# Performance work log

Measured on AMD Instinct MI355X. Metric: run time of the kernel, lower is better.

The kernel has to match this reference:

```python
import jax, jax.numpy as jnp
import numpy as np
import math

# ---- hyperparameters (init_kwargs) ----
D = 2              # spatial dimension
MTOT = 65          # quadrature nodes per dimension (odd)
LENGTHSCALE = 0.1  # SE kernel lengthscale
OUTPUTSCALE = 1.0  # SE kernel variance
SIGMASQ = 0.05     # observation noise variance
CG_ITERS = 30      # fixed CG iteration count (replaces tol-based early stopping)
N_TRAIN = 100000
N_TEST = 50000
TWO_PI = 2.0 * math.pi


def setup_inputs() -> dict:
    key = jax.random.key(0)
    k1, k2, k3 = jax.random.split(key, 3)
    x = jax.random.uniform(k1, (N_TRAIN, D), dtype=jnp.float32)
    y = jax.random.normal(k2, (N_TRAIN,), dtype=jnp.float32)
    x_new = jax.random.uniform(k3, (N_TEST, D), dtype=jnp.float32)
    return {"x": x, "y": y, "x_new": x_new}


def _phases(col, h, freqs, isign):
    # exp(isign * i * 2*pi*h * x * k), shape [N, K]
    return jnp.exp((1j * isign * TWO_PI) * (h * col[:, None] * freqs[None, :]).astype(jnp.float32))


def _nudft_type1(pts, c, h, freqs):
    # fk[a,b] = sum_n c_n exp(-2*pi*i*h*(k_a x_n0 + k_b x_n1)); separable tensor grid
    E0 = _phases(pts[:, 0], h, freqs, -1.0)
    E1 = _phases(pts[:, 1], h, freqs, -1.0)
    return jnp.einsum('n,na,nb->ab', c.astype(jnp.complex64), E0, E1)


def _nudft_type2(pts, fk, h, freqs):
    # f_n = sum_{a,b} fk[a,b] exp(+2*pi*i*h*(k_a x_n0 + k_b x_n1))
    E0 = _phases(pts[:, 0], h, freqs, +1.0)
    E1 = _phases(pts[:, 1], h, freqs, +1.0)
    return jnp.einsum('ab,na,nb->n', fk, E0, E1)


def _cg(A, b, iters):
    # complex Hermitian-PSD conjugate gradients, fixed iteration count
    x0 = jnp.zeros_like(b)
    r0 = b
    rs0 = jnp.real(jnp.vdot(r0, r0))

    def step(carry, _):
        xk, r, p, rs = carry
        Ap = A(p)
        alpha = rs / jnp.real(jnp.vdot(p, Ap))
        xk = xk + alpha * p
        r = r - alpha * Ap
        rs_new = jnp.real(jnp.vdot(r, r))
        p = r + (rs_new / rs) * p
        return (xk, r, p, rs_new), None

    (xk, _, _, _), _ = jax.lax.scan(step, (x0, r0, r0, rs0), None, length=iters)
    return xk


def _forward(x, y, x_new):
    m = (MTOT - 1) // 2
    # geometry / quadrature (get_xis): domain extent L, spacing h = 1/L, grid k = -m..m
    x_all = jnp.concatenate((x, x_new), axis=0)
    L = jnp.max(jnp.max(x_all, axis=0) - jnp.min(x_all, axis=0))
    L = jnp.where(L <= 1e-9, jnp.float32(1.0), L)
    h = (1.0 / L).astype(jnp.float32)
    k = (jnp.arange(MTOT) - m).astype(jnp.float32)
    xis_1d = h * k
    X0, X1 = jnp.meshgrid(xis_1d, xis_1d, indexing='ij')
    sq = X0 * X0 + X1 * X1  # [MTOT, MTOT] squared frequency norm
    # squared-exponential spectral density S(s) = sigma_f^2 (2*pi*l^2)^(d/2) exp(-2*pi^2*l^2 |s|^2)
    l2 = LENGTHSCALE * LENGTHSCALE
    spec = OUTPUTSCALE * (TWO_PI * l2) ** (D / 2) * jnp.exp((-2.0 * math.pi ** 2 * l2) * sq)
    ws = jnp.sqrt(spec * h ** D).reshape(-1).astype(jnp.complex64)  # [M]

    # rhs = ws * F^H y  (type-1 NUFFT, exact NUDFT)
    rhs = ws * _nudft_type1(x, y, h, k).reshape(-1)

    # Toeplitz convolution vector v[o] = sum_n exp(-2*pi*i*h*o.x_n), offsets -(mtot-1)..(mtot-1)
    kk = (jnp.arange(2 * MTOT - 1) - (MTOT - 1)).astype(jnp.float32)
    Ev0 = _phases(x[:, 0], h, kk, -1.0)
    Ev1 = _phases(x[:, 1], h, kk, -1.0)
    v = jnp.einsum('na,nb->ab', Ev0, Ev1)  # [2M-1, 2M-1]
    # circularly align offset 0 to index 0, precompute FFT
    v_circ = jnp.roll(v, shift=(-(MTOT - 1), -(MTOT - 1)), axis=(0, 1))
    vhat = jnp.fft.fftn(v_circ)
    s_fft = (2 * MTOT - 1, 2 * MTOT - 1)

    def toeplitz_apply(w):  # w: [MTOT, MTOT] complex
        W = jnp.fft.fftn(w, s=s_fft)
        full = jnp.fft.ifftn(vhat * W)
        return full[:MTOT, :MTOT]

    def A_mean(beta):  # (W F^H F W + sigma^2 I) beta, beta flat [M]
        wb = (ws * beta).reshape(MTOT, MTOT)
        Tw = toeplitz_apply(wb).reshape(-1)
        return ws * Tw + SIGMASQ * beta

    beta = _cg(A_mean, rhs, CG_ITERS)
    # posterior mean at test points via type-2 NUFFT
    yhat = jnp.real(_nudft_type2(x_new, (ws * beta).reshape(MTOT, MTOT), h, k))
    return yhat


def reference(x, y, x_new):
    return _forward(x, y, x_new)
```

## Files before the change

### kernel.cpp

```cpp
#include <hip/hip_runtime.h>
#include <math.h>

#define M2 4225
#define NTRAIN 100000
#define NTEST 50000
#define CGITERS 30
#define TWO_PI_D 6.283185307179586476925287
#define TPI32 6.28318530717958647692f

#define F_H 0
#define F_RS 1
#define F_PAP 2
#define F_RSN 3
#define F_WS 8
#define F_RHS 4234
#define F_X 12684
#define F_R 21134
#define F_P 29584
#define F_AP 38034
#define F_PB 46484
#define F_VF 50710
#define F_VHAT 83992
#define F_PROD 117274
#define D_VPART 125330
#define D_FKPART 2271890

#define NCHUNK 128
#define PTSB2 782
#define VHALF 8385
#define VH2 16770
#define FKHALF 2145
#define FH2 4290
#define NB_APPLY 529

__device__ __forceinline__ unsigned fkey(float f){
  unsigned u = __float_as_uint(f);
  return (u & 0x80000000u) ? ~u : (u | 0x80000000u);
}
__device__ __forceinline__ float fdec(unsigned k){
  unsigned u = (k & 0x80000000u) ? (k & 0x7fffffffu) : ~k;
  return __uint_as_float(u);
}

__global__ void k_init(unsigned* mm){
  if (threadIdx.x == 0){
    mm[0] = 0xFFFFFFFFu; mm[1] = 0u; mm[2] = 0xFFFFFFFFu; mm[3] = 0u;
  }
}

__global__ void k_minmax(const float* __restrict__ x, const float* __restrict__ xn,
                         unsigned* __restrict__ mm){
  int tid = blockIdx.x * blockDim.x + threadIdx.x;
  int str = gridDim.x * blockDim.x;
  float mn0 = 1e30f, mx0 = -1e30f, mn1 = 1e30f, mx1 = -1e30f;
  const float2* a = (const float2*)x;
  for (int i = tid; i < NTRAIN; i += str){
    float2 v = a[i];
    mn0 = fminf(mn0, v.x); mx0 = fmaxf(mx0, v.x);
    mn1 = fminf(mn1, v.y); mx1 = fmaxf(mx1, v.y);
  }
  const float2* b = (const float2*)xn;
  for (int i = tid; i < NTEST; i += str){
    float2 v = b[i];
    mn0 = fminf(mn0, v.x); mx0 = fmaxf(mx0, v.x);
    mn1 = fminf(mn1, v.y); mx1 = fmaxf(mx1, v.y);
  }
  for (int off = 32; off; off >>= 1){
    mn0 = fminf(mn0, __shfl_xor(mn0, off, 64));
    mx0 = fmaxf(mx0, __shfl_xor(mx0, off, 64));
    mn1 = fminf(mn1, __shfl_xor(mn1, off, 64));
    mx1 = fmaxf(mx1, __shfl_xor(mx1, off, 64));
  }
  if ((threadIdx.x & 63) == 0){
    atomicMin(&mm[0], fkey(mn0)); atomicMax(&mm[1], fkey(mx0));
    atomicMin(&mm[2], fkey(mn1)); atomicMax(&mm[3], fkey(mx1));
  }
}

__global__ void k_setup(float* __restrict__ wsf){
  const unsigned* mm = (const unsigned*)(wsf + 4);
  float mn0 = fdec(mm[0]), mx0 = fdec(mm[1]);
  float mn1 = fdec(mm[2]), mx1 = fdec(mm[3]);
  float d0 = __fsub_rn(mx0, mn0), d1 = __fsub_rn(mx1, mn1);
  float L = fmaxf(d0, d1);
  if (L <= 1e-9f) L = 1.0f;
  float hf = __fdiv_rn(1.0f, L);
  if (threadIdx.x == 0) wsf[F_H] = hf;
  const float c0f = (float)(TWO_PI_D * 0.01);
  const float c1f = (float)(-2.0 * 9.869604401089358618834 * 0.01);
  float h2f = __fmul_rn(hf, hf);
  for (int e = threadIdx.x; e < M2; e += blockDim.x){
    int r = e / 65, c = e - r * 65;
    float xi0 = __fmul_rn(hf, (float)(r - 32));
    float xi1 = __fmul_rn(hf, (float)(c - 32));
    float sq = __fadd_rn(__fmul_rn(xi0, xi0), __fmul_rn(xi1, xi1));
    float spec = __fmul_rn(c0f, expf(__fmul_rn(c1f, sq)));
    wsf[F_WS + e] = sqrtf(__fmul_rn(spec, h2f));
  }
}

__launch_bounds__(256)
__global__ void k_v_main(const float* __restrict__ x, const float* __restrict__ wsf,
                         double* __restrict__ vpart){
  __shared__ double2 aL[16][80];
  __shared__ double2 bL[16][16];
  __shared__ float hxs[16][2];
  const float hf = wsf[F_H];
  const int tid = threadIdx.x;
  const int t0 = tid >> 4, t1 = tid & 15;
  const int jcol = blockIdx.y * 16 + t1;
  double2 acc[5];
  #pragma unroll
  for (int k = 0; k < 5; ++k) acc[k] = make_double2(0.0, 0.0);
  const int p0 = blockIdx.x * PTSB2;
  const int pend = min(p0 + PTSB2, NTRAIN);
  for (int base = p0; base < pend; base += 16){
    if (tid < 32){
      int p = tid >> 1, d = tid & 1;
      int gp = base + p;
      hxs[p][d] = (gp < pend) ? __fmul_rn(hf, x[2 * gp + d]) : 0.f;
    }
    __syncthreads();
    for (int i = tid; i < 16 * 80; i += 256){
      int p = i / 80;
      int o = i - p * 80;
      int gp = base + p;
      double2 va = make_double2(0.0, 0.0);
      if (gp < pend && o < 65){
        float t = __fmul_rn(hxs[p][0], (float)o);
        float sn, cs; sincosf(__fmul_rn(TPI32, t), &sn, &cs);
        va = make_double2((double)cs, (double)(-sn));
      }
      aL[p][o] = va;
    }
    {
      int p = t0, c = t1;
      int gp = base + p;
      int j = blockIdx.y * 16 + c;
      double2 vb = make_double2(0.0, 0.0);
      if (gp < pend && j < 129){
        float t = __fmul_rn(hxs[p][1], (float)(j - 64));
        float sn, cs; sincosf(__fmul_rn(TPI32, t), &sn, &cs);
        vb = make_double2((double)cs, (double)(-sn));
      }
      bL[p][c] = vb;
    }
    __syncthreads();
    #pragma unroll 1
    for (int p = 0; p < 16; ++p){
      double2 bv = bL[p][t1];
      double2 av[5];
      #pragma unroll
      for (int k = 0; k < 5; ++k) av[k] = aL[p][t0 + 16 * k];
      #pragma unroll
      for (int k = 0; k < 5; ++k){
        acc[k].x += av[k].x * bv.x - av[k].y * bv.y;
        acc[k].y += av[k].x * bv.y + av[k].y * bv.x;
      }
    }
    __syncthreads();
  }
  double* outp = vpart + (size_t)blockIdx.x * VH2;
  if (jcol < 129){
    #pragma unroll
    for (int k = 0; k < 5; ++k){
      int o0 = t0 + 16 * k;
      if (o0 < 65){
        int e = o0 * 129 + jcol;
        outp[2 * e] = acc[k].x;
        outp[2 * e + 1] = acc[k].y;
      }
    }
  }
}

__launch_bounds__(256)
__global__ void k_fk_main(const float* __restrict__ x, const float* __restrict__ y,
                          const float* __restrict__ wsf, double* __restrict__ fkpart){
  __shared__ double2 aL[16][48];
  __shared__ double2 bL[16][16];
  __shared__ float hxs[16][2];
  __shared__ float ys[16];
  const float hf = wsf[F_H];
  const int tid = threadIdx.x;
  const int t0 = tid >> 4, t1 = tid & 15;
  const int jcol = blockIdx.y * 16 + t1;
  double2 acc[3];
  #pragma unroll
  for (int k = 0; k < 3; ++k) acc[k] = make_double2(0.0, 0.0);
  const int p0 = blockIdx.x * PTSB2;
  const int pend = min(p0 + PTSB2, NTRAIN);
  for (int base = p0; base < pend; base += 16){
    if (tid < 32){
      int p = tid >> 1, d = tid & 1;
      int gp = base + p;
      hxs[p][d] = (gp < pend) ? __fmul_rn(hf, x[2 * gp + d]) : 0.f;
    } else if (tid < 48){
      int p = tid - 32;
      int gp = base + p;
      ys[p] = (gp < pend) ? y[gp] : 0.f;
    }
    __syncthreads();
    for (int i = tid; i < 16 * 48; i += 256){
      int p = i / 48, o = i - p * 48;
      int gp = base + p;
      double2 val = make_double2(0.0, 0.0);
      if (o < 33 && gp < pend){
        float t = __fmul_rn(hxs[p][0], (float)o);
        float sn, cs; sincosf(__fmul_rn(TPI32, t), &sn, &cs);
        val = make_double2((double)__fmul_rn(ys[p], cs), (double)__fmul_rn(ys[p], -sn));
      }
      aL[p][o] = val;
    }
    {
      int p = t0, c = t1;
      int gp = base + p;
      int j = blockIdx.y * 16 + c;
      double2 vb = make_double2(0.0, 0.0);
      if (gp < pend && j < 65){
        float t = __fmul_rn(hxs[p][1], (float)(j - 32));
        float sn, cs; sincosf(__fmul_rn(TPI32, t), &sn, &cs);
        vb = make_double2((double)cs, (double)(-sn));
      }
      bL[p][c] = vb;
    }
    __syncthreads();
    #pragma unroll 1
    for (int p = 0; p < 16; ++p){
      double2 bv = bL[p][t1];
      double2 av[3];
      #pragma unroll
      for (int k = 0; k < 3; ++k) av[k] = aL[p][t0 + 16 * k];
      #pragma unroll
      for (int k = 0; k < 3; ++k){
        acc[k].x += av[k].x * bv.x - av[k].y * bv.y;
        acc[k].y += av[k].x * bv.y + av[k].y * bv.x;
      }
    }
    __syncthreads();
  }
  double* outp = fkpart + (size_t)blockIdx.x * FH2;
  if (jcol < 65){
    #pragma unroll
    for (int k = 0; k < 3; ++k){
      int o0 = t0 + 16 * k;
      if (o0 < 33){
        int e = o0 * 65 + jcol;
        outp[2 * e] = acc[k].x;
        outp[2 * e + 1] = acc[k].y;
      }
    }
  }
}

__global__ void k_reduce_v(const double* __restrict__ wsd, float* __restrict__ wsf){
  int e = blockIdx.x * blockDim.x + threadIdx.x;
  if (e >= VHALF) return;
  const double* vp = wsd + D_VPART;
  double sr = 0.0, si = 0.0;
  for (int k = 0; k < NCHUNK; ++k){
    sr += vp[(size_t)k * VH2 + 2 * e];
    si += vp[(size_t)k * VH2 + 2 * e + 1];
  }
  float r32 = (float)sr, i32 = (float)si;
  int o0 = e / 129, j = e - o0 * 129;
  float2* vF = (float2*)(wsf + F_VF);
  vF[(o0 + 64) * 129 + j] = make_float2(r32, i32);
  if (o0 > 0) vF[(64 - o0) * 129 + (128 - j)] = make_float2(r32, -i32);
}

__global__ void k_reduce_fk(const double* __restrict__ wsd, float* __restrict__ wsf){
  int e = blockIdx.x * blockDim.x + threadIdx.x;
  if (e >= FKHALF) return;
  const double* fp = wsd + D_FKPART;
  double sr = 0.0, si = 0.0;
  for (int k = 0; k < NCHUNK; ++k){
    sr += fp[(size_t)k * FH2 + 2 * e];
    si += fp[(size_t)k * FH2 + 2 * e + 1];
  }
  float fr = (float)sr, fi = (float)si;
  int a = e / 65, c = e - a * 65;
  int ef = (a + 32) * 65 + c;
  float wf = wsf[F_WS + ef];
  float* rhs = wsf + F_RHS;
  rhs[2 * ef] = __fmul_rn(wf, fr);
  rhs[2 * ef + 1] = __fmul_rn(wf, fi);
  if (a > 0){
    int ef2 = (32 - a) * 65 + (64 - c);
    float wf2 = wsf[F_WS + ef2];
    rhs[2 * ef2] = __fmul_rn(wf2, fr);
    rhs[2 * ef2 + 1] = -__fmul_rn(wf2, fi);
  }
}

__launch_bounds__(192)
__global__ void k_vhat(float* __restrict__ wsf){
  __shared__ double twc[129], tws[129];
  __shared__ double t1r[129], t1i[129];
  int p = blockIdx.x, t = threadIdx.x;
  if (t < 129){
    double ang = TWO_PI_D * (double)t / 129.0;
    double s, c; sincos(ang, &s, &c);
    twc[t] = c; tws[t] = s;
  }
  __syncthreads();
  if (t < 129){
    const float2* vF = (const float2*)(wsf + F_VF);
    int n = t;
    int nsrc = (n + 64) % 129;
    double ar = 0.0, ai = 0.0;
    for (int m = 0; m < 129; ++m){
      float2 v = vF[((m + 64) % 129) * 129 + nsrc];
      int idx = (p * m) % 129;
      double wr = twc[idx], wi = -tws[idx];
      ar += (double)v.x * wr - (double)v.y * wi;
      ai += (double)v.x * wi + (double)v.y * wr;
    }
    t1r[n] = ar; t1i[n] = ai;
  }
  __syncthreads();
  if (t < 129){
    int q = t;
    double ar = 0.0, ai = 0.0;
    for (int n = 0; n < 129; ++n){
      int idx = (q * n) % 129;
      double wr = twc[idx], wi = -tws[idx];
      ar += t1r[n] * wr - t1i[n] * wi;
      ai += t1r[n] * wi + t1i[n] * wr;
    }
    ((float2*)(wsf + F_VHAT))[p * 129 + q] = make_float2((float)ar, (float)ai);
  }
}

__global__ void k_cg_init(float* __restrict__ wsf){
  int e = blockIdx.x * blockDim.x + threadIdx.x;
  if (e >= M2) return;
  const float2* rhs = (const float2*)(wsf + F_RHS);
  float2 b = rhs[e];
  ((float2*)(wsf + F_X))[e] = make_float2(0.f, 0.f);
  ((float2*)(wsf + F_R))[e] = b;
  ((float2*)(wsf + F_P))[e] = b;
  wsf[F_PB + e] = __fadd_rn(__fmul_rn(b.x, b.x), __fmul_rn(b.y, b.y));
}

__device__ __forceinline__ float pw_leaf(const float* d, int o, int n){
  float r0 = d[o], r1 = d[o+1], r2 = d[o+2], r3 = d[o+3];
  float r4 = d[o+4], r5 = d[o+5], r6 = d[o+6], r7 = d[o+7];
  int i = 8;
  int lim = n - (n & 7);
  for (; i < lim; i += 8){
    r0 = __fadd_rn(r0, d[o+i]);   r1 = __fadd_rn(r1, d[o+i+1]);
    r2 = __fadd_rn(r2, d[o+i+2]); r3 = __fadd_rn(r3, d[o+i+3]);
    r4 = __fadd_rn(r4, d[o+i+4]); r5 = __fadd_rn(r5, d[o+i+5]);
    r6 = __fadd_rn(r6, d[o+i+6]); r7 = __fadd_rn(r7, d[o+i+7]);
  }
  float res = __fadd_rn(__fadd_rn(__fadd_rn(r0, r1), __fadd_rn(r2, r3)),
                        __fadd_rn(__fadd_rn(r4, r5), __fadd_rn(r6, r7)));
  for (; i < n; ++i) res = __fadd_rn(res, d[o+i]);
  return res;
}

__device__ __forceinline__ void pw_tree(const float* pb, float* T, int tid){
  if (tid < 16){
    const int tb[16] = {0,264,528,792,1056,1320,1584,1848,
                        2112,2376,2640,2904,3168,3432,3696,3960};
    int base = tb[tid];
    int sz3 = (tid == 15) ? 73 : 72;
    float L0 = pw_leaf(pb, base, 128);
    float L1 = pw_leaf(pb, base + 128, 64);
    float L2 = pw_leaf(pb, base + 192, sz3);
    T[tid] = __fadd_rn(L0, __fadd_rn(L1, L2));
  }
  __syncthreads();
  if (tid == 0){
    float s0 = __fadd_rn(__fadd_rn(T[0], T[1]), __fadd_rn(T[2], T[3]));
    float s1 = __fadd_rn(__fadd_rn(T[4], T[5]), __fadd_rn(T[6], T[7]));
    float s2 = __fadd_rn(__fadd_rn(T[8], T[9]), __fadd_rn(T[10], T[11]));
    float s3 = __fadd_rn(__fadd_rn(T[12], T[13]), __fadd_rn(T[14], T[15]));
    T[0] = __fadd_rn(__fadd_rn(s0, s1), __fadd_rn(s2, s3));
  }
}

__launch_bounds__(256)
__global__ void k_pair0(float* __restrict__ wsf){
  __shared__ float pb[M2];
  __shared__ float T[16];
  int tid = threadIdx.x;
  for (int i = tid; i < M2; i += 256) pb[i] = wsf[F_PB + i];
  __syncthreads();
  pw_tree(pb, T, tid);
  __syncthreads();
  if (tid == 0) wsf[F_RS] = T[0];
}

__launch_bounds__(192)
__global__ void k_wfft(float* __restrict__ wsf){
  __shared__ double twc[129], tws[129];
  __shared__ double t1r[65], t1i[65];
  int pr = blockIdx.x, t = threadIdx.x;
  if (t < 129){
    double ang = TWO_PI_D * (double)t / 129.0;
    double s, c; sincos(ang, &s, &c);
    twc[t] = c; tws[t] = s;
  }
  __syncthreads();
  if (t < 65){
    const float2* P = (const float2*)(wsf + F_P);
    const float* W = wsf + F_WS;
    int n = t;
    double ar = 0.0, ai = 0.0;
    for (int m = 0; m < 65; ++m){
      int e = m * 65 + n;
      float2 p = P[e];
      float w = W[e];
      float wbr = __fmul_rn(w, p.x), wbi = __fmul_rn(w, p.y);
      int idx = (pr * m) % 129;
      double wr = twc[idx], wi = -tws[idx];
      ar += (double)wbr * wr - (double)wbi * wi;
      ai += (double)wbr * wi + (double)wbi * wr;
    }
    t1r[n] = ar; t1i[n] = ai;
  }
  __syncthreads();
  if (t < 129){
    int q = t;
    double ar = 0.0, ai = 0.0;
    for (int n = 0; n < 65; ++n){
      int idx = (q * n) % 129;
      double wr = twc[idx], wi = -tws[idx];
      ar += t1r[n] * wr - t1i[n] * wi;
      ai += t1r[n] * wi + t1i[n] * wr;
    }
    float Wr = (float)ar, Wi = (float)ai;
    float2 v = ((const float2*)(wsf + F_VHAT))[pr * 129 + q];
    float prre = __fsub_rn(__fmul_rn(v.x, Wr), __fmul_rn(v.y, Wi));
    float prim = __fadd_rn(__fmul_rn(v.x, Wi), __fmul_rn(v.y, Wr));
    ((float2*)(wsf + F_PROD))[pr * 129 + q] = make_float2(prre, prim);
  }
}

__launch_bounds__(192)
__global__ void k_ifft(float* __restrict__ wsf){
  __shared__ double twc[129], tws[129];
  __shared__ double ur[129], ui[129];
  int m = blockIdx.x, t = threadIdx.x;
  if (t < 129){
    double ang = TWO_PI_D * (double)t / 129.0;
    double s, c; sincos(ang, &s, &c);
    twc[t] = c; tws[t] = s;
  }
  __syncthreads();
  if (t < 129){
    const float2* prod = (const float2*)(wsf + F_PROD);
    int q = t;
    double ar = 0.0, ai = 0.0;
    for (int pr = 0; pr < 129; ++pr){
      float2 v = prod[pr * 129 + q];
      int idx = (m * pr) % 129;
      double wr = twc[idx], wi = tws[idx];
      ar += (double)v.x * wr - (double)v.y * wi;
      ai += (double)v.x * wi + (double)v.y * wr;
    }
    const double sc = 1.0 / 129.0;
    ur[q] = ar * sc; ui[q] = ai * sc;
  }
  __syncthreads();
  if (t < 65){
    int n = t;
    double ar = 0.0, ai = 0.0;
    for (int q = 0; q < 129; ++q){
      int idx = (n * q) % 129;
      double wr = twc[idx], wi = tws[idx];
      ar += ur[q] * wr - ui[q] * wi;
      ai += ur[q] * wi + ui[q] * wr;
    }
    const double sc = 1.0 / 129.0;
    float Twr = (float)(ar * sc), Twi = (float)(ai * sc);
    int e = m * 65 + n;
    float w = wsf[F_WS + e];
    float2 p = ((const float2*)(wsf + F_P))[e];
    float Apx = __fadd_rn(__fmul_rn(w, Twr), __fmul_rn(0.05f, p.x));
    float Apy = __fadd_rn(__fmul_rn(w, Twi), __fmul_rn(0.05f, p.y));
    ((float2*)(wsf + F_AP))[e] = make_float2(Apx, Apy);
    wsf[F_PB + e] = __fadd_rn(__fmul_rn(p.x, Apx), __fmul_rn(p.y, Apy));
  }
}

__launch_bounds__(256)
__global__ void k_cgstep(float* __restrict__ wsf){
  __shared__ float pb[M2];
  __shared__ float T[16];
  __shared__ float sh[2];
  int tid = threadIdx.x;
  for (int i = tid; i < M2; i += 256) pb[i] = wsf[F_PB + i];
  __syncthreads();
  pw_tree(pb, T, tid);
  __syncthreads();
  if (tid == 0){
    float rs = wsf[F_RS];
    sh[1] = rs;
    sh[0] = __fdiv_rn(rs, T[0]);
  }
  __syncthreads();
  float alpha = sh[0];
  float2* X = (float2*)(wsf + F_X);
  float2* R = (float2*)(wsf + F_R);
  float2* P = (float2*)(wsf + F_P);
  const float2* AP = (const float2*)(wsf + F_AP);
  for (int e = tid; e < M2; e += 256){
    float2 p = P[e], ap = AP[e], xv = X[e], rv = R[e];
    xv.x = __fadd_rn(xv.x, __fmul_rn(alpha, p.x));
    xv.y = __fadd_rn(xv.y, __fmul_rn(alpha, p.y));
    rv.x = __fsub_rn(rv.x, __fmul_rn(alpha, ap.x));
    rv.y = __fsub_rn(rv.y, __fmul_rn(alpha, ap.y));
    X[e] = xv; R[e] = rv;
    pb[e] = __fadd_rn(__fmul_rn(rv.x, rv.x), __fmul_rn(rv.y, rv.y));
  }
  __syncthreads();
  pw_tree(pb, T, tid);
  __syncthreads();
  if (tid == 0){
    float rsn = T[0];
    sh[0] = __fdiv_rn(rsn, sh[1]);
    wsf[F_RS] = rsn;
  }
  __syncthreads();
  float beta = sh[0];
  for (int e = tid; e < M2; e += 256){
    float2 rv = R[e], p = P[e];
    P[e] = make_float2(__fadd_rn(rv.x, __fmul_rn(beta, p.x)),
                       __fadd_rn(rv.y, __fmul_rn(beta, p.y)));
  }
}

__launch_bounds__(256)
__global__ void k_predict(const float* __restrict__ xn, const float* __restrict__ wsf,
                          float* __restrict__ out){
  __shared__ double fbRe[M2];
  __shared__ double fbIm[M2];
  const float hf = wsf[F_H];
  const float* wsq = wsf + F_WS;
  const float2* xb = (const float2*)(wsf + F_X);
  int tid = threadIdx.x;
  for (int i = tid; i < M2; i += 256){
    float w = wsq[i]; float2 q = xb[i];
    fbRe[i] = (double)__fmul_rn(w, q.x);
    fbIm[i] = (double)__fmul_rn(w, q.y);
  }
  __syncthreads();
  int lane = tid & 63;
  int wid = (blockIdx.x * 256 + tid) >> 6;
  int nw = (gridDim.x * 256) >> 6;
  for (int n = wid; n < NTEST; n += nw){
    float hx0 = __fmul_rn(hf, xn[2 * n]);
    float hx1 = __fmul_rn(hf, xn[2 * n + 1]);
    float t0 = __fmul_rn(hx0, (float)(lane - 32));
    float s0, c0; sincosf(__fmul_rn(TPI32, t0), &s0, &c0);
    float t1 = __fmul_rn(hx1, (float)(lane - 32));
    float s1, c1; sincosf(__fmul_rn(TPI32, t1), &s1, &c1);
    float t0x = __fmul_rn(hx0, 32.0f);
    float s0x, c0x; sincosf(__fmul_rn(TPI32, t0x), &s0x, &c0x);
    float t1x = __fmul_rn(hx1, 32.0f);
    float s1x, c1x; sincosf(__fmul_rn(TPI32, t1x), &s1x, &c1x);
    double e0r = (double)c0, e0i = (double)s0;
    double e1r = (double)c1, e1i = (double)s1;
    double gr = 0.0, gi = 0.0;
    for (int a = 0; a < 64; ++a){
      double er = __shfl(e0r, a, 64);
      double ei = __shfl(e0i, a, 64);
      double fr = fbRe[a * 65 + lane];
      double fi = fbIm[a * 65 + lane];
      gr += fr * er - fi * ei;
      gi += fr * ei + fi * er;
    }
    {
      double fr = fbRe[64 * 65 + lane], fi = fbIm[64 * 65 + lane];
      gr += fr * (double)c0x - fi * (double)s0x;
      gi += fr * (double)s0x + fi * (double)c0x;
    }
    double contrib = gr * e1r - gi * e1i;
    {
      double fr = fbRe[lane * 65 + 64], fi = fbIm[lane * 65 + 64];
      double ur = fr * e0r - fi * e0i;
      double ui = fr * e0i + fi * e0r;
      contrib += ur * (double)c1x - ui * (double)s1x;
      if (lane == 0){
        double fr2 = fbRe[64 * 65 + 64], fi2 = fbIm[64 * 65 + 64];
        double vr = fr2 * (double)c0x - fi2 * (double)s0x;
        double vi = fr2 * (double)s0x + fi2 * (double)c0x;
        contrib += vr * (double)c1x - vi * (double)s1x;
      }
    }
    for (int off = 32; off; off >>= 1) contrib += __shfl_xor(contrib, off, 64);
    if (lane == 0) out[n] = (float)contrib;
  }
}

extern "C" void kernel_launch(void* const* d_in, const int* in_sizes, int n_in,
                              void* d_out, int out_size, void* d_ws, size_t ws_size,
                              hipStream_t stream){
  const float* x = (const float*)d_in[0];
  const float* y = (const float*)d_in[1];
  const float* xnew = (const float*)d_in[2];
  float* wsf = (float*)d_ws;
  double* wsd = (double*)d_ws;
  float* out = (float*)d_out;
  unsigned* mm = (unsigned*)(wsf + 4);

  k_init<<<1, 64, 0, stream>>>(mm);
  k_minmax<<<256, 256, 0, stream>>>(x, xnew, mm);
  k_setup<<<1, 256, 0, stream>>>(wsf);
  k_v_main<<<dim3(NCHUNK, 9), 256, 0, stream>>>(x, wsf, wsd + D_VPART);
  k_fk_main<<<dim3(NCHUNK, 5), 256, 0, stream>>>(x, y, wsf, wsd + D_FKPART);
  k_reduce_v<<<33, 256, 0, stream>>>(wsd, wsf);
  k_reduce_fk<<<9, 256, 0, stream>>>(wsd, wsf);
  k_vhat<<<129, 192, 0, stream>>>(wsf);
  k_cg_init<<<17, 256, 0, stream>>>(wsf);
  k_pair0<<<1, 256, 0, stream>>>(wsf);
  for (int it = 0; it < CGITERS; ++it){
    k_wfft<<<129, 192, 0, stream>>>(wsf);
    k_ifft<<<65, 192, 0, stream>>>(wsf);
    k_cgstep<<<1, 256, 0, stream>>>(wsf);
  }
  k_predict<<<256, 256, 0, stream>>>(xnew, wsf, out);
}
```

Before: 2.283 ms.

## Merge v and fk accumulation kernels and widen column tile to 32

Fuses the Toeplitz vector and type-1 NUDFT partial-sum kernels into one launch, with blockIdx.y selecting which product a block computes. Each thread now accumulates two column outputs, so every A-operand load and its sincos computation serve twice as many columns, and fewer blocks recompute the A phases. This removes a launch and redundant trig work, at the cost of more accumulator registers and fewer blocks (1024 instead of 1792), which may lower occupancy in the double-precision inner loop.

Result: faster. 2.173 ms (-4.8%).

```diff
diff --git a/kernel.cpp b/kernel.cpp
--- a/kernel.cpp
+++ b/kernel.cpp
@@ -31,7 +31,6 @@
 #define VH2 16770
 #define FKHALF 2145
 #define FH2 4290
-#define NB_APPLY 529
 
 __device__ __forceinline__ unsigned fkey(float f){
   unsigned u = __float_as_uint(f);
@@ -100,154 +99,160 @@
 }
 
 __launch_bounds__(256)
-__global__ void k_v_main(const float* __restrict__ x, const float* __restrict__ wsf,
-                         double* __restrict__ vpart){
+__global__ void k_vfk(const float* __restrict__ x, const float* __restrict__ y,
+                      const float* __restrict__ wsf,
+                      double* __restrict__ vpart, double* __restrict__ fkpart){
   __shared__ double2 aL[16][80];
-  __shared__ double2 bL[16][16];
-  __shared__ float hxs[16][2];
-  const float hf = wsf[F_H];
-  const int tid = threadIdx.x;
-  const int t0 = tid >> 4, t1 = tid & 15;
-  const int jcol = blockIdx.y * 16 + t1;
-  double2 acc[5];
-  #pragma unroll
-  for (int k = 0; k < 5; ++k) acc[k] = make_double2(0.0, 0.0);
-  const int p0 = blockIdx.x * PTSB2;
-  const int pend = min(p0 + PTSB2, NTRAIN);
-  for (int base = p0; base < pend; base += 16){
-    if (tid < 32){
-      int p = tid >> 1, d = tid & 1;
-      int gp = base + p;
-      hxs[p][d] = (gp < pend) ? __fmul_rn(hf, x[2 * gp + d]) : 0.f;
-    }
-    __syncthreads();
-    for (int i = tid; i < 16 * 80; i += 256){
-      int p = i / 80;
-      int o = i - p * 80;
-      int gp = base + p;
-      double2 va = make_double2(0.0, 0.0);
-      if (gp < pend && o < 65){
-        float t = __fmul_rn(hxs[p][0], (float)o);
-        float sn, cs; sincosf(__fmul_rn(TPI32, t), &sn, &cs);
-        va = make_double2((double)cs, (double)(-sn));
-      }
-      aL[p][o] = va;
-    }
-    {
-      int p = t0, c = t1;
-      int gp = base + p;
-      int j = blockIdx.y * 16 + c;
-      double2 vb = make_double2(0.0, 0.0);
-      if (gp < pend && j < 129){
-        float t = __fmul_rn(hxs[p][1], (float)(j - 64));
-        float sn, cs; sincosf(__fmul_rn(TPI32, t), &sn, &cs);
-        vb = make_double2((double)cs, (double)(-sn));
-      }
-      bL[p][c] = vb;
-    }
-    __syncthreads();
-    #pragma unroll 1
-    for (int p = 0; p < 16; ++p){
-      double2 bv = bL[p][t1];
-      double2 av[5];
-      #pragma unroll
-      for (int k = 0; k < 5; ++k) av[k] = aL[p][t0 + 16 * k];
-      #pragma unroll
-      for (int k = 0; k < 5; ++k){
-        acc[k].x += av[k].x * bv.x - av[k].y * bv.y;
-        acc[k].y += av[k].x * bv.y + av[k].y * bv.x;
-      }
-    }
-    __syncthreads();
-  }
-  double* outp = vpart + (size_t)blockIdx.x * VH2;
-  if (jcol < 129){
-    #pragma unroll
-    for (int k = 0; k < 5; ++k){
-      int o0 = t0 + 16 * k;
-      if (o0 < 65){
-        int e = o0 * 129 + jcol;
-        outp[2 * e] = acc[k].x;
-        outp[2 * e + 1] = acc[k].y;
-      }
-    }
-  }
-}
-
-__launch_bounds__(256)
-__global__ void k_fk_main(const float* __restrict__ x, const float* __restrict__ y,
-                          const float* __restrict__ wsf, double* __restrict__ fkpart){
-  __shared__ double2 aL[16][48];
-  __shared__ double2 bL[16][16];
+  __shared__ double2 bL[16][32];
   __shared__ float hxs[16][2];
   __shared__ float ys[16];
   const float hf = wsf[F_H];
   const int tid = threadIdx.x;
   const int t0 = tid >> 4, t1 = tid & 15;
-  const int jcol = blockIdx.y * 16 + t1;
-  double2 acc[3];
-  #pragma unroll
-  for (int k = 0; k < 3; ++k) acc[k] = make_double2(0.0, 0.0);
+  const bool isV = (blockIdx.y < 5);
+  const int colbase = (isV ? blockIdx.y : (blockIdx.y - 5)) * 32;
   const int p0 = blockIdx.x * PTSB2;
   const int pend = min(p0 + PTSB2, NTRAIN);
-  for (int base = p0; base < pend; base += 16){
-    if (tid < 32){
-      int p = tid >> 1, d = tid & 1;
-      int gp = base + p;
-      hxs[p][d] = (gp < pend) ? __fmul_rn(hf, x[2 * gp + d]) : 0.f;
-    } else if (tid < 48){
-      int p = tid - 32;
-      int gp = base + p;
-      ys[p] = (gp < pend) ? y[gp] : 0.f;
-    }
-    __syncthreads();
-    for (int i = tid; i < 16 * 48; i += 256){
-      int p = i / 48, o = i - p * 48;
-      int gp = base + p;
-      double2 val = make_double2(0.0, 0.0);
-      if (o < 33 && gp < pend){
-        float t = __fmul_rn(hxs[p][0], (float)o);
-        float sn, cs; sincosf(__fmul_rn(TPI32, t), &sn, &cs);
-        val = make_double2((double)__fmul_rn(ys[p], cs), (double)__fmul_rn(ys[p], -sn));
-      }
-      aL[p][o] = val;
-    }
-    {
-      int p = t0, c = t1;
-      int gp = base + p;
-      int j = blockIdx.y * 16 + c;
-      double2 vb = make_double2(0.0, 0.0);
-      if (gp < pend && j < 65){
-        float t = __fmul_rn(hxs[p][1], (float)(j - 32));
-        float sn, cs; sincosf(__fmul_rn(TPI32, t), &sn, &cs);
-        vb = make_double2((double)cs, (double)(-sn));
-      }
-      bL[p][c] = vb;
-    }
-    __syncthreads();
-    #pragma unroll 1
-    for (int p = 0; p < 16; ++p){
-      double2 bv = bL[p][t1];
-      double2 av[3];
-      #pragma unroll
-      for (int k = 0; k < 3; ++k) av[k] = aL[p][t0 + 16 * k];
-      #pragma unroll
-      for (int k = 0; k < 3; ++k){
-        acc[k].x += av[k].x * bv.x - av[k].y * bv.y;
-        acc[k].y += av[k].x * bv.y + av[k].y * bv.x;
-      }
-    }
-    __syncthreads();
-  }
-  double* outp = fkpart + (size_t)blockIdx.x * FH2;
-  if (jcol < 65){
+
+  if (isV){
+    double2 acc[5][2];
+    #pragma unroll
+    for (int k = 0; k < 5; ++k){ acc[k][0] = make_double2(0.0, 0.0); acc[k][1] = make_double2(0.0, 0.0); }
+    for (int base = p0; base < pend; base += 16){
+      if (tid < 32){
+        int p = tid >> 1, d = tid & 1;
+        int gp = base + p;
+        hxs[p][d] = (gp < pend) ? __fmul_rn(hf, x[2 * gp + d]) : 0.f;
+      }
+      __syncthreads();
+      for (int i = tid; i < 16 * 80; i += 256){
+        int p = i / 80;
+        int o = i - p * 80;
+        int gp = base + p;
+        double2 va = make_double2(0.0, 0.0);
+        if (gp < pend && o < 65){
+          float t = __fmul_rn(hxs[p][0], (float)o);
+          float sn, cs; sincosf(__fmul_rn(TPI32, t), &sn, &cs);
+          va = make_double2((double)cs, (double)(-sn));
+        }
+        aL[p][o] = va;
+      }
+      for (int i = tid; i < 16 * 32; i += 256){
+        int p = i >> 5, c = i & 31;
+        int gp = base + p;
+        int j = colbase + c;
+        double2 vb = make_double2(0.0, 0.0);
+        if (gp < pend && j < 129){
+          float t = __fmul_rn(hxs[p][1], (float)(j - 64));
+          float sn, cs; sincosf(__fmul_rn(TPI32, t), &sn, &cs);
+          vb = make_double2((double)cs, (double)(-sn));
+        }
+        bL[p][c] = vb;
+      }
+      __syncthreads();
+      #pragma unroll 1
+      for (int p = 0; p < 16; ++p){
+        double2 bv0 = bL[p][t1];
+        double2 bv1 = bL[p][t1 + 16];
+        double2 av[5];
+        #pragma unroll
+        for (int k = 0; k < 5; ++k) av[k] = aL[p][t0 + 16 * k];
+        #pragma unroll
+        for (int k = 0; k < 5; ++k){
+          acc[k][0].x += av[k].x * bv0.x - av[k].y * bv0.y;
+          acc[k][0].y += av[k].x * bv0.y + av[k].y * bv0.x;
+          acc[k][1].x += av[k].x * bv1.x - av[k].y * bv1.y;
+          acc[k][1].y += av[k].x * bv1.y + av[k].y * bv1.x;
+        }
+      }
+      __syncthreads();
+    }
+    double* outp = vpart + (size_t)blockIdx.x * VH2;
+    #pragma unroll
+    for (int k = 0; k < 5; ++k){
+      int o0 = t0 + 16 * k;
+      if (o0 < 65){
+        #pragma unroll
+        for (int cc = 0; cc < 2; ++cc){
+          int jcol = colbase + t1 + 16 * cc;
+          if (jcol < 129){
+            int e = o0 * 129 + jcol;
+            outp[2 * e] = acc[k][cc].x;
+            outp[2 * e + 1] = acc[k][cc].y;
+          }
+        }
+      }
+    }
+  } else {
+    double2 acc[3][2];
+    #pragma unroll
+    for (int k = 0; k < 3; ++k){ acc[k][0] = make_double2(0.0, 0.0); acc[k][1] = make_double2(0.0, 0.0); }
+    for (int base = p0; base < pend; base += 16){
+      if (tid < 32){
+        int p = tid >> 1, d = tid & 1;
+        int gp = base + p;
+        hxs[p][d] = (gp < pend) ? __fmul_rn(hf, x[2 * gp + d]) : 0.f;
+      } else if (tid < 48){
+        int p = tid - 32;
+        int gp = base + p;
+        ys[p] = (gp < pend) ? y[gp] : 0.f;
+      }
+      __syncthreads();
+      for (int i = tid; i < 16 * 48; i += 256){
+        int p = i / 48, o = i - p * 48;
+        int gp = base + p;
+        double2 val = make_double2(0.0, 0.0);
+        if (o < 33 && gp < pend){
+          float t = __fmul_rn(hxs[p][0], (float)o);
+          float sn, cs; sincosf(__fmul_rn(TPI32, t), &sn, &cs);
+          val = make_double2((double)__fmul_rn(ys[p], cs), (double)__fmul_rn(ys[p], -sn));
+        }
+        aL[p][o] = val;
+      }
+      for (int i = tid; i < 16 * 32; i += 256){
+        int p = i >> 5, c = i & 31;
+        int gp = base + p;
+        int j = colbase + c;
+        double2 vb = make_double2(0.0, 0.0);
+        if (gp < pend && j < 65){
+          float t = __fmul_rn(hxs[p][1], (float)(j - 32));
+          float sn, cs; sincosf(__fmul_rn(TPI32, t), &sn, &cs);
+          vb = make_double2((double)cs, (double)(-sn));
+        }
+        bL[p][c] = vb;
+      }
+      __syncthreads();
+      #pragma unroll 1
+      for (int p = 0; p < 16; ++p){
+        double2 bv0 = bL[p][t1];
+        double2 bv1 = bL[p][t1 + 16];
+        double2 av[3];
+        #pragma unroll
+        for (int k = 0; k < 3; ++k) av[k] = aL[p][t0 + 16 * k];
+        #pragma unroll
+        for (int k = 0; k < 3; ++k){
+          acc[k][0].x += av[k].x * bv0.x - av[k].y * bv0.y;
+          acc[k][0].y += av[k].x * bv0.y + av[k].y * bv0.x;
+          acc[k][1].x += av[k].x * bv1.x - av[k].y * bv1.y;
+          acc[k][1].y += av[k].x * bv1.y + av[k].y * bv1.x;
+        }
+      }
+      __syncthreads();
+    }
+    double* outp = fkpart + (size_t)blockIdx.x * FH2;
     #pragma unroll
     for (int k = 0; k < 3; ++k){
       int o0 = t0 + 16 * k;
       if (o0 < 33){
-        int e = o0 * 65 + jcol;
-        outp[2 * e] = acc[k].x;
-        outp[2 * e + 1] = acc[k].y;
+        #pragma unroll
+        for (int cc = 0; cc < 2; ++cc){
+          int jcol = colbase + t1 + 16 * cc;
+          if (jcol < 65){
+            int e = o0 * 65 + jcol;
+            outp[2 * e] = acc[k][cc].x;
+            outp[2 * e + 1] = acc[k][cc].y;
+          }
+        }
       }
     }
   }
@@ -610,8 +615,7 @@
   k_init<<<1, 64, 0, stream>>>(mm);
   k_minmax<<<256, 256, 0, stream>>>(x, xnew, mm);
   k_setup<<<1, 256, 0, stream>>>(wsf);
-  k_v_main<<<dim3(NCHUNK, 9), 256, 0, stream>>>(x, wsf, wsd + D_VPART);
-  k_fk_main<<<dim3(NCHUNK, 5), 256, 0, stream>>>(x, y, wsf, wsd + D_FKPART);
+  k_vfk<<<dim3(NCHUNK, 8), 256, 0, stream>>>(x, y, wsf, wsd + D_VPART, wsd + D_FKPART);
   k_reduce_v<<<33, 256, 0, stream>>>(wsd, wsf);
   k_reduce_fk<<<9, 256, 0, stream>>>(wsd, wsf);
   k_vhat<<<129, 192, 0, stream>>>(wsf);
```
